# Kernel tuning notes

Hardware: AMD Instinct MI355X
Metric: run time of the kernel (lower is better)

## Reference

```python
import jax, jax.numpy as jnp
import numpy as np

# Each of the 16 soft logic gates in tableOperator is a polynomial
#   gate_t(A,B) = c0 + cA*A + cB*B + cAB*A*B
# _COEFF[t] = [c0, cA, cB, cAB], matching the torch tableOperator rows 0..15.
_COEFF = np.array([
    [0,  0,  0,  0],   # 0: 0
    [0,  0,  0,  1],   # 1: A*B
    [0,  1,  0, -1],   # 2: A - A*B
    [0,  1,  0,  0],   # 3: A
    [0,  0,  1, -1],   # 4: B - A*B
    [0,  0,  1,  0],   # 5: B
    [0,  1,  1, -2],   # 6: A + B - 2AB
    [0,  1,  1, -1],   # 7: A + B - AB
    [1, -1, -1,  1],   # 8: 1 - (A + B - AB)
    [1, -1, -1,  2],   # 9: 1 - (A + B - 2AB)
    [1,  0, -1,  0],   # 10: 1 - B
    [1,  0, -1,  1],   # 11: 1 - B + AB
    [1, -1,  0,  0],   # 12: 1 - A
    [1, -1,  0,  1],   # 13: 1 - A + AB
    [1,  0,  0, -1],   # 14: 1 - AB
    [1,  0,  0,  0],   # 15: 1
], dtype=np.float32)

PREV_SIZE, SIZE, BATCH = 2048, 2048, 8192

def setup_inputs() -> dict:
    key = jax.random.key(0)
    k1, k2, k3, k4 = jax.random.split(key, 4)
    return {
        "prev_layer_output": jax.random.uniform(k1, (PREV_SIZE, BATCH), dtype=jnp.float32),
        "input_A_weights": jax.random.normal(k2, (SIZE, PREV_SIZE), dtype=jnp.float32) * 0.05,
        "input_B_weights": jax.random.normal(k3, (SIZE, PREV_SIZE), dtype=jnp.float32) * 0.05,
        "table_weights": jax.random.normal(k4, (16, SIZE), dtype=jnp.float32) * 0.05,
    }

def reference(prev_layer_output, input_A_weights, input_B_weights, table_weights):
    # Training (grad-enabled) path of LogicLayer.forward; GradFactor(x, 1) is identity.
    pA = jax.nn.softmax(input_A_weights, axis=1)   # [size, prev_size]
    pB = jax.nn.softmax(input_B_weights, axis=1)   # [size, prev_size]
    pT = jax.nn.softmax(table_weights, axis=0)     # [16, size]
    A = pA @ prev_layer_output                     # [size, batch]
    B = pB @ prev_layer_output                     # [size, batch]
    # Fuse sum_t pT[t] * gate_t(A,B): contract gate coefficients with table probs.
    c = jnp.einsum('tc,ts->cs', jnp.asarray(_COEFF), pT)  # [4, size]
    out = (c[0][:, None]
           + c[1][:, None] * A
           + c[2][:, None] * B
           + c[3][:, None] * (A * B))               # [size, batch]
    return out
```

## Files before the change

kernel.cpp:

```cpp
#include <hip/hip_runtime.h>
#include <hip/hip_bf16.h>

#define M_DIM 2048
#define K_DIM 2048
#define N_DIM 8192

#define BM 128
#define BN 128
#define BK 64
#define NT (K_DIM / BK)

typedef __attribute__((ext_vector_type(4))) int i32x4;

static __device__ __forceinline__ void stage1k(const unsigned char* g, void* l) {
    __builtin_amdgcn_global_load_lds(
        (const __attribute__((address_space(1))) void*)g,
        (__attribute__((address_space(3))) void*)l, 16, 0, 0);
}

__global__ __launch_bounds__(256) void prep_kernel(
    const float* __restrict__ prev, const float* __restrict__ Wa,
    const float* __restrict__ Wb, const float* __restrict__ TW,
    unsigned char* __restrict__ Pa, unsigned char* __restrict__ Pb,
    unsigned char* __restrict__ Pt,
    float* __restrict__ SA, float* __restrict__ SB, float4* __restrict__ C4)
{
    __shared__ unsigned char tile[64][80];
    __shared__ float redm[4], reds[4];
    const int bx = blockIdx.x;
    const int t = threadIdx.x;

    if (bx < 4096) {
        const int n0 = (bx & 127) * 64;
        const int k0 = (bx >> 7) * 64;
        const int kb = (t >> 4) * 4;
        const int nb = (t & 15) * 4;
        unsigned int pk0 = 0, pk1 = 0, pk2 = 0, pk3 = 0;
#pragma unroll
        for (int j = 0; j < 4; ++j) {
            float4 v = *(const float4*)(prev + (size_t)(k0 + kb + j) * N_DIM + n0 + nb);
            pk0 |= (unsigned int)(unsigned char)(int)(127.f * v.x + 0.5f) << (8 * j);
            pk1 |= (unsigned int)(unsigned char)(int)(127.f * v.y + 0.5f) << (8 * j);
            pk2 |= (unsigned int)(unsigned char)(int)(127.f * v.z + 0.5f) << (8 * j);
            pk3 |= (unsigned int)(unsigned char)(int)(127.f * v.w + 0.5f) << (8 * j);
        }
        *(unsigned int*)&tile[nb + 0][kb] = pk0;
        *(unsigned int*)&tile[nb + 1][kb] = pk1;
        *(unsigned int*)&tile[nb + 2][kb] = pk2;
        *(unsigned int*)&tile[nb + 3][kb] = pk3;
        __syncthreads();
        const int n = t >> 2;
        const int k16 = (t & 3) * 16;
        int4 v = *(const int4*)&tile[n][k16];
        *(int4*)(Pt + (size_t)(n0 + n) * K_DIM + k0 + k16) = v;
        return;
    }
    if (bx < 8192) {
        const int r = bx - 4096;
        const int row = r & 2047;
        const int isB = r >> 11;
        const float* W = isB ? Wb : Wa;
        unsigned char* P = isB ? Pb : Pa;
        float* S = isB ? SB : SA;
        const float* w = W + (size_t)row * K_DIM + t * 8;
        float4 v0 = *(const float4*)(w);
        float4 v1 = *(const float4*)(w + 4);
        float x[8] = {v0.x, v0.y, v0.z, v0.w, v1.x, v1.y, v1.z, v1.w};

        float m = x[0];
#pragma unroll
        for (int i = 1; i < 8; ++i) m = fmaxf(m, x[i]);
#pragma unroll
        for (int off = 32; off >= 1; off >>= 1) m = fmaxf(m, __shfl_xor(m, off));
        const int wid = t >> 6;
        if ((t & 63) == 0) redm[wid] = m;
        __syncthreads();
        m = fmaxf(fmaxf(redm[0], redm[1]), fmaxf(redm[2], redm[3]));

        float s = 0.f;
#pragma unroll
        for (int i = 0; i < 8; ++i) { x[i] = __expf(x[i] - m); s += x[i]; }
#pragma unroll
        for (int off = 32; off >= 1; off >>= 1) s += __shfl_xor(s, off);
        if ((t & 63) == 0) reds[wid] = s;
        __syncthreads();
        s = reds[0] + reds[1] + reds[2] + reds[3];

        union { unsigned char u[8]; int2 v; } pk;
#pragma unroll
        for (int i = 0; i < 8; ++i)
            pk.u[i] = (unsigned char)(int)(127.f * x[i] + 0.5f);
        *(int2*)(P + (size_t)row * K_DIM + t * 8) = pk.v;
        if (t == 0) S[row] = 1.f / (16129.f * s);
        return;
    }
    const int s = (bx - 8192) * 256 + t;
    if (s >= M_DIM) return;
    float x[16];
    float m = -1e30f;
#pragma unroll
    for (int tt = 0; tt < 16; ++tt) { x[tt] = TW[tt * M_DIM + s]; m = fmaxf(m, x[tt]); }
    float sum = 0.f;
#pragma unroll
    for (int tt = 0; tt < 16; ++tt) { x[tt] = __expf(x[tt] - m); sum += x[tt]; }
    const float inv = 1.0f / sum;
    const float c0a[16] = {0,0,0,0,0,0,0,0, 1,1,1,1,1,1,1,1};
    const float cAa[16] = {0,0,1,1,0,0,1,1, -1,-1,0,0,-1,-1,0,0};
    const float cBa[16] = {0,0,0,0,1,1,1,1, -1,-1,-1,-1,0,0,0,0};
    const float cXa[16] = {0,1,-1,0,-1,0,-2,-1, 1,2,0,1,0,1,-1,0};
    float c0 = 0.f, cA = 0.f, cB = 0.f, cX = 0.f;
#pragma unroll
    for (int tt = 0; tt < 16; ++tt) {
        const float p = x[tt] * inv;
        c0 += p * c0a[tt]; cA += p * cAa[tt]; cB += p * cBa[tt]; cX += p * cXa[tt];
    }
    C4[s] = make_float4(c0, cA, cB, cX);
}


#define MFMA8(ACC, FA, FP, MI0)                                                \
    _Pragma("unroll") for (int mi = (MI0); mi < (MI0) + 2; ++mi)               \
    _Pragma("unroll") for (int ni = 0; ni < 4; ++ni)                           \
        ACC[mi][ni] = __builtin_amdgcn_mfma_i32_16x16x64_i8(                   \
            FA[mi], FP[ni], ACC[mi][ni], 0, 0, 0);

#define STAGE(T) do { const int b_ = (T) % 3;                                  \
    const size_t o_ = (size_t)(T) * BK;                                        \
    stage1k(gPa + o_,               &sPa[b_][wid * 16][0]);                    \
    stage1k(gPa + o_ + 64 * K_DIM,  &sPa[b_][64 + wid * 16][0]);               \
    stage1k(gPb + o_,               &sPb[b_][wid * 16][0]);                    \
    stage1k(gPb + o_ + 64 * K_DIM,  &sPb[b_][64 + wid * 16][0]);               \
    stage1k(gPt + o_,               &sPt[b_][wid * 16][0]);                    \
    stage1k(gPt + o_ + 64 * K_DIM,  &sPt[b_][64 + wid * 16][0]); } while (0)

__global__ __launch_bounds__(256, 2) void logic_gemm_kernel(
    const unsigned char* __restrict__ Pa,
    const unsigned char* __restrict__ Pb,
    const unsigned char* __restrict__ Pt,
    const float4* __restrict__ C4,
    const float* __restrict__ SA,
    const float* __restrict__ SB,
    float* __restrict__ out)
{
    __shared__ unsigned char sPa[3][128][64];
    __shared__ unsigned char sPb[3][128][64];
    __shared__ unsigned char sPt[3][128][64];

    const int m0 = blockIdx.y * BM;
    const int n0 = blockIdx.x * BN;
    const int t = threadIdx.x;
    const int wid = t >> 6, lane = t & 63;
    const int wr = wid >> 1, wc = wid & 1;
    const int lq = lane >> 4, lr = lane & 15;

    const int srow = lane >> 2;
    const int scol = (((lane & 3) ^ ((lane >> 3) & 3)) << 4);
    const unsigned char* gPa = Pa + (size_t)(m0 + wid * 16 + srow) * K_DIM + scol;
    const unsigned char* gPb = Pb + (size_t)(m0 + wid * 16 + srow) * K_DIM + scol;
    const unsigned char* gPt = Pt + (size_t)(n0 + wid * 16 + srow) * K_DIM + scol;

    const int cswz = (lq ^ ((lr >> 1) & 3)) << 4;
    const int roA = (wr * 64 + lr) * 64 + cswz;
    const int roP = (wc * 64 + lr) * 64 + cswz;

    i32x4 accA[4][4] = {};
    i32x4 accB[4][4] = {};
    i32x4 fa[4], fb[4], fp[4];

    STAGE(0);
    STAGE(1);
    asm volatile("s_waitcnt vmcnt(6)" ::: "memory");
    __builtin_amdgcn_s_barrier();

    for (int kt = 0; kt < NT; ++kt) {
        const int bcur = kt % 3;
        const char* bA = (const char*)&sPa[bcur][0][0];
        const char* bB = (const char*)&sPb[bcur][0][0];
        const char* bP = (const char*)&sPt[bcur][0][0];

        if (kt + 2 < NT) STAGE(kt + 2);

#pragma unroll
        for (int i = 0; i < 4; ++i) fa[i] = *(const i32x4*)(bA + roA + i * 1024);
#pragma unroll
        for (int i = 0; i < 4; ++i) fp[i] = *(const i32x4*)(bP + roP + i * 1024);
#pragma unroll
        for (int i = 0; i < 4; ++i) fb[i] = *(const i32x4*)(bB + roA + i * 1024);

        __builtin_amdgcn_s_setprio(1);
        MFMA8(accA, fa, fp, 0);
        MFMA8(accA, fa, fp, 2);
        MFMA8(accB, fb, fp, 0);
        MFMA8(accB, fb, fp, 2);
        __builtin_amdgcn_s_setprio(0);

        if (kt < NT - 2) asm volatile("s_waitcnt vmcnt(6)" ::: "memory");
        else             asm volatile("s_waitcnt vmcnt(0)" ::: "memory");
        __builtin_amdgcn_s_barrier();
    }

#pragma unroll
    for (int mi = 0; mi < 4; ++mi) {
#pragma unroll
        for (int i = 0; i < 4; ++i) {
            const int row = m0 + wr * 64 + mi * 16 + lq * 4 + i;
            const float4 c = C4[row];
            const float sa = SA[row];
            const float sb = SB[row];
#pragma unroll
            for (int ni = 0; ni < 4; ++ni) {
                const int col = n0 + wc * 64 + ni * 16 + lr;
                const float Av = (float)accA[mi][ni][i] * sa;
                const float Bv = (float)accB[mi][ni][i] * sb;
                out[(size_t)row * N_DIM + col] = c.x + c.y * Av + c.z * Bv + c.w * Av * Bv;
            }
        }
    }
}

extern "C" void kernel_launch(void* const* d_in, const int* in_sizes, int n_in,
                              void* d_out, int out_size, void* d_ws, size_t ws_size,
                              hipStream_t stream) {
    const float* prev = (const float*)d_in[0];
    const float* Wa   = (const float*)d_in[1];
    const float* Wb   = (const float*)d_in[2];
    const float* TW   = (const float*)d_in[3];
    float* out = (float*)d_out;

    char* ws = (char*)d_ws;
    unsigned char* Pa = (unsigned char*)(ws);
    unsigned char* Pb = (unsigned char*)(ws + (size_t)(4u << 20));
    unsigned char* Pt = (unsigned char*)(ws + (size_t)(8u << 20));
    float4* C4 = (float4*)(ws + (size_t)(24u << 20));
    float*  SA = (float*)(ws + (size_t)(24u << 20) + (32u << 10));
    float*  SB = (float*)(ws + (size_t)(24u << 20) + (64u << 10));

    prep_kernel<<<dim3(8200), 256, 0, stream>>>(prev, Wa, Wb, TW,
                                                Pa, Pb, Pt, SA, SB, C4);
    logic_gemm_kernel<<<dim3(N_DIM / BN, M_DIM / BM), 256, 0, stream>>>(Pa, Pb, Pt, C4, SA, SB, out);
}
```

Baseline: 96.35 us.

## Widen N tile to 256 with 4-stage LDS pipeline and fragment double-buffering

Doubles the block's N tile so each workgroup computes a 128x256 output and reuses the A and B fragments across twice as many MFMAs. The LDS ring grows from three to four buffers, so loads run three tiles ahead. Register fragments are double-buffered so the next tile's LDS reads are interleaved between the A and B MFMA batches, hiding LDS latency. The cost is larger register and LDS use, which forces occupancy to one workgroup per CU. That raises the risk of spills and leaves fewer waves to hide latency.

```diff
diff --git a/kernel.cpp b/kernel.cpp
--- a/kernel.cpp
+++ b/kernel.cpp
@@ -6,7 +6,7 @@
 #define N_DIM 8192
 
 #define BM 128
-#define BN 128
+#define BN 256
 #define BK 64
 #define NT (K_DIM / BK)
 
@@ -118,22 +118,49 @@
 }
 
 
-#define MFMA8(ACC, FA, FP, MI0)                                                \
-    _Pragma("unroll") for (int mi = (MI0); mi < (MI0) + 2; ++mi)               \
-    _Pragma("unroll") for (int ni = 0; ni < 4; ++ni)                           \
+#define MFMA32(ACC, FX, FP)                                                    \
+    _Pragma("unroll") for (int mi = 0; mi < 4; ++mi)                           \
+    _Pragma("unroll") for (int ni = 0; ni < 8; ++ni)                           \
         ACC[mi][ni] = __builtin_amdgcn_mfma_i32_16x16x64_i8(                   \
-            FA[mi], FP[ni], ACC[mi][ni], 0, 0, 0);
-
-#define STAGE(T) do { const int b_ = (T) % 3;                                  \
-    const size_t o_ = (size_t)(T) * BK;                                        \
-    stage1k(gPa + o_,               &sPa[b_][wid * 16][0]);                    \
-    stage1k(gPa + o_ + 64 * K_DIM,  &sPa[b_][64 + wid * 16][0]);               \
-    stage1k(gPb + o_,               &sPb[b_][wid * 16][0]);                    \
-    stage1k(gPb + o_ + 64 * K_DIM,  &sPb[b_][64 + wid * 16][0]);               \
-    stage1k(gPt + o_,               &sPt[b_][wid * 16][0]);                    \
-    stage1k(gPt + o_ + 64 * K_DIM,  &sPt[b_][64 + wid * 16][0]); } while (0)
-
-__global__ __launch_bounds__(256, 2) void logic_gemm_kernel(
+            FX[mi], FP[ni], ACC[mi][ni], 0, 0, 0);
+
+#define STAGE(T, B) do { const size_t o_ = (size_t)(T) * BK;                   \
+    stage1k(gPa + o_,                &sPa[B][wid * 16][0]);                    \
+    stage1k(gPa + o_ + 64 * K_DIM,   &sPa[B][64 + wid * 16][0]);               \
+    stage1k(gPb + o_,                &sPb[B][wid * 16][0]);                    \
+    stage1k(gPb + o_ + 64 * K_DIM,   &sPb[B][64 + wid * 16][0]);               \
+    stage1k(gPt + o_,                &sPt[B][wid * 16][0]);                    \
+    stage1k(gPt + o_ + 64 * K_DIM,   &sPt[B][64 + wid * 16][0]);               \
+    stage1k(gPt + o_ + 128 * K_DIM,  &sPt[B][128 + wid * 16][0]);              \
+    stage1k(gPt + o_ + 192 * K_DIM,  &sPt[B][192 + wid * 16][0]); } while (0)
+
+#define READ_FRAGS(FA, FB, FP, B) do {                                         \
+    const char* bA_ = (const char*)&sPa[B][0][0];                              \
+    const char* bB_ = (const char*)&sPb[B][0][0];                              \
+    const char* bP_ = (const char*)&sPt[B][0][0];                              \
+    _Pragma("unroll") for (int i = 0; i < 4; ++i)                              \
+        FA[i] = *(const i32x4*)(bA_ + roA + i * 1024);                         \
+    _Pragma("unroll") for (int i = 0; i < 4; ++i)                              \
+        FB[i] = *(const i32x4*)(bB_ + roA + i * 1024);                         \
+    _Pragma("unroll") for (int i = 0; i < 8; ++i)                              \
+        FP[i] = *(const i32x4*)(bP_ + roP + i * 1024);                         \
+} while (0)
+
+#define KT_STEP(KT, BJ, FA_C, FB_C, FP_C, FA_N, FB_N, FP_N) do {               \
+    if ((KT) + 3 < NT) STAGE((KT) + 3, (((BJ) + 3) & 3));                      \
+    __builtin_amdgcn_s_setprio(1);                                             \
+    MFMA32(accA, FA_C, FP_C);                                                  \
+    __builtin_amdgcn_s_setprio(0);                                             \
+    if ((KT) + 1 < NT) READ_FRAGS(FA_N, FB_N, FP_N, (((BJ) + 1) & 3));         \
+    __builtin_amdgcn_s_setprio(1);                                             \
+    MFMA32(accB, FB_C, FP_C);                                                  \
+    __builtin_amdgcn_s_setprio(0);                                             \
+    if ((KT) < NT - 3) asm volatile("s_waitcnt vmcnt(8)" ::: "memory");        \
+    else               asm volatile("s_waitcnt vmcnt(0)" ::: "memory");        \
+    __builtin_amdgcn_s_barrier();                                              \
+} while (0)
+
+__global__ __launch_bounds__(256, 1) void logic_gemm_kernel(
     const unsigned char* __restrict__ Pa,
     const unsigned char* __restrict__ Pb,
     const unsigned char* __restrict__ Pt,
@@ -142,9 +169,9 @@
     const float* __restrict__ SB,
     float* __restrict__ out)
 {
-    __shared__ unsigned char sPa[3][128][64];
-    __shared__ unsigned char sPb[3][128][64];
-    __shared__ unsigned char sPt[3][128][64];
+    __shared__ unsigned char sPa[4][128][64];
+    __shared__ unsigned char sPb[4][128][64];
+    __shared__ unsigned char sPt[4][256][64];
 
     const int m0 = blockIdx.y * BM;
     const int n0 = blockIdx.x * BN;
@@ -161,42 +188,23 @@
 
     const int cswz = (lq ^ ((lr >> 1) & 3)) << 4;
     const int roA = (wr * 64 + lr) * 64 + cswz;
-    const int roP = (wc * 64 + lr) * 64 + cswz;
-
-    i32x4 accA[4][4] = {};
-    i32x4 accB[4][4] = {};
-    i32x4 fa[4], fb[4], fp[4];
-
-    STAGE(0);
-    STAGE(1);
-    asm volatile("s_waitcnt vmcnt(6)" ::: "memory");
+    const int roP = (wc * 128 + lr) * 64 + cswz;
+
+    i32x4 accA[4][8] = {};
+    i32x4 accB[4][8] = {};
+    i32x4 faE[4], fbE[4], fpE[8], faO[4], fbO[4], fpO[8];
+
+    STAGE(0, 0); STAGE(1, 1); STAGE(2, 2);
+    asm volatile("s_waitcnt vmcnt(8)" ::: "memory");
     __builtin_amdgcn_s_barrier();
-
-    for (int kt = 0; kt < NT; ++kt) {
-        const int bcur = kt % 3;
-        const char* bA = (const char*)&sPa[bcur][0][0];
-        const char* bB = (const char*)&sPb[bcur][0][0];
-        const char* bP = (const char*)&sPt[bcur][0][0];
-
-        if (kt + 2 < NT) STAGE(kt + 2);
-
-#pragma unroll
-        for (int i = 0; i < 4; ++i) fa[i] = *(const i32x4*)(bA + roA + i * 1024);
-#pragma unroll
-        for (int i = 0; i < 4; ++i) fp[i] = *(const i32x4*)(bP + roP + i * 1024);
-#pragma unroll
-        for (int i = 0; i < 4; ++i) fb[i] = *(const i32x4*)(bB + roA + i * 1024);
-
-        __builtin_amdgcn_s_setprio(1);
-        MFMA8(accA, fa, fp, 0);
-        MFMA8(accA, fa, fp, 2);
-        MFMA8(accB, fb, fp, 0);
-        MFMA8(accB, fb, fp, 2);
-        __builtin_amdgcn_s_setprio(0);
-
-        if (kt < NT - 2) asm volatile("s_waitcnt vmcnt(6)" ::: "memory");
-        else             asm volatile("s_waitcnt vmcnt(0)" ::: "memory");
-        __builtin_amdgcn_s_barrier();
+    READ_FRAGS(faE, fbE, fpE, 0);
+
+    for (int it = 0; it < NT / 4; ++it) {
+        const int kt = it * 4;
+        KT_STEP(kt + 0, 0, faE, fbE, fpE, faO, fbO, fpO);
+        KT_STEP(kt + 1, 1, faO, fbO, fpO, faE, fbE, fpE);
+        KT_STEP(kt + 2, 2, faE, fbE, fpE, faO, fbO, fpO);
+        KT_STEP(kt + 3, 3, faO, fbO, fpO, faE, fbE, fpE);
     }
 
 #pragma unroll
@@ -208,8 +216,8 @@
             const float sa = SA[row];
             const float sb = SB[row];
 #pragma unroll
-            for (int ni = 0; ni < 4; ++ni) {
-                const int col = n0 + wc * 64 + ni * 16 + lr;
+            for (int ni = 0; ni < 8; ++ni) {
+                const int col = n0 + wc * 128 + ni * 16 + lr;
                 const float Av = (float)accA[mi][ni][i] * sa;
                 const float Bv = (float)accB[mi][ni][i] * sb;
                 out[(size_t)row * N_DIM + col] = c.x + c.y * Av + c.z * Bv + c.w * Av * Bv;
```

Measured after the change: 95.50 us. Within noise of the previous version (-0.9%).
